# Optimization experiments

Measured on AMD Instinct MI355X. Metric: run time of the kernel, lower is better.

The kernel has to match this reference:

```python
import jax, jax.numpy as jnp
import numpy as np

B, C, H, W = 8, 320, 32, 32
HEADS, DHEAD = 8, 40
CTX_LEN, CTX_DIM = 77, 768
FF_INNER = 4 * C
GROUPS = 32
HW = H * W


def setup_inputs() -> dict:
    key = jax.random.key(0)
    ks = jax.random.split(key, 16)
    def nrm(k, shape, s=0.02):
        return (jax.random.normal(k, shape) * s).astype(jnp.float32)
    z = lambda *s: jnp.zeros(s, jnp.float32)
    o = lambda *s: jnp.ones(s, jnp.float32)
    inp = {}
    inp["x"] = jax.random.normal(ks[0], (B, C, H, W), jnp.float32)
    inp["context"] = jax.random.normal(ks[1], (B, CTX_LEN, CTX_DIM), jnp.float32)
    inp["vis_mask"] = jax.random.uniform(ks[2], (B, HW, HW)) > 0.5
    inp["v2t_mask"] = jax.random.uniform(ks[3], (B, HW, CTX_LEN)) > 0.5
    inp["gn_scale"] = o(C); inp["gn_bias"] = z(C)
    inp["proj_in_w"] = nrm(ks[4], (C, C)); inp["proj_in_b"] = z(C)
    inp["n1_s"] = o(C); inp["n1_b"] = z(C)
    inp["wq1"] = nrm(ks[5], (C, C)); inp["wk1"] = nrm(ks[6], (C, C)); inp["wv1"] = nrm(ks[7], (C, C))
    inp["wo1"] = nrm(ks[8], (C, C)); inp["bo1"] = z(C)
    inp["n2_s"] = o(C); inp["n2_b"] = z(C)
    inp["wq2"] = nrm(ks[9], (C, C)); inp["wk2"] = nrm(ks[10], (CTX_DIM, C)); inp["wv2"] = nrm(ks[11], (CTX_DIM, C))
    inp["wo2"] = nrm(ks[12], (C, C)); inp["bo2"] = z(C)
    inp["n3_s"] = o(C); inp["n3_b"] = z(C)
    inp["ff_w1"] = nrm(ks[13], (C, 2 * FF_INNER)); inp["ff_b1"] = z(2 * FF_INNER)
    inp["ff_w2"] = nrm(ks[14], (FF_INNER, C)); inp["ff_b2"] = z(C)
    inp["proj_out_w"] = nrm(ks[15], (C, C)); inp["proj_out_b"] = z(C)
    return inp


def group_norm(x, scale, bias, eps=1e-6):
    b, c, h, w = x.shape
    xg = x.reshape(b, GROUPS, -1)
    mu = xg.mean(-1, keepdims=True)
    var = xg.var(-1, keepdims=True)
    xn = ((xg - mu) * jax.lax.rsqrt(var + eps)).reshape(b, c, h, w)
    return xn * scale[None, :, None, None] + bias[None, :, None, None]


def layer_norm(x, s, b, eps=1e-5):
    mu = x.mean(-1, keepdims=True)
    var = x.var(-1, keepdims=True)
    return (x - mu) * jax.lax.rsqrt(var + eps) * s + b


def mha(xq, ctx, wq, wk, wv, wo, bo, mask):
    # CrossAttention: manual einsum softmax with boolean mask broadcast over heads
    b, n, _ = xq.shape
    m = ctx.shape[1]
    split = lambda t: t.reshape(b, -1, HEADS, DHEAD).transpose(0, 2, 1, 3)
    q = split(xq @ wq)   # [b,h,n,d]
    k = split(ctx @ wk)  # [b,h,m,d]
    v = split(ctx @ wv)
    sim = jnp.einsum('bhid,bhjd->bhij', q, k) * (DHEAD ** -0.5)
    if mask is not None:
        sim = jnp.where(mask[:, None, :, :], sim, jnp.finfo(sim.dtype).min)
    attn = jax.nn.softmax(sim, axis=-1)
    out = jnp.einsum('bhij,bhjd->bhid', attn, v)
    out = out.transpose(0, 2, 1, 3).reshape(b, n, HEADS * DHEAD)
    return out @ wo + bo


def reference(x, context, vis_mask, v2t_mask, gn_scale, gn_bias, proj_in_w, proj_in_b,
              n1_s, n1_b, wq1, wk1, wv1, wo1, bo1,
              n2_s, n2_b, wq2, wk2, wv2, wo2, bo2,
              n3_s, n3_b, ff_w1, ff_b1, ff_w2, ff_b2,
              proj_out_w, proj_out_b):
    x_in = x
    h = group_norm(x, gn_scale, gn_bias)
    # 1x1 conv proj_in == per-pixel linear; flatten b c h w -> b (hw) c
    h = h.reshape(B, C, HW).transpose(0, 2, 1) @ proj_in_w + proj_in_b
    # masked self-attention (vis mask)
    h = h + mha(layer_norm(h, n1_s, n1_b), layer_norm(h, n1_s, n1_b),
                wq1, wk1, wv1, wo1, bo1, vis_mask)
    # masked cross-attention to text (v2t mask)
    h = h + mha(layer_norm(h, n2_s, n2_b), context,
                wq2, wk2, wv2, wo2, bo2, v2t_mask)
    # GEGLU feedforward (glu=True, mult=4)
    y = layer_norm(h, n3_s, n3_b) @ ff_w1 + ff_b1
    a, g = jnp.split(y, 2, axis=-1)
    h = h + (a * jax.nn.gelu(g, approximate=False)) @ ff_w2 + ff_b2
    # proj_out + residual
    out = (h @ proj_out_w + proj_out_b).transpose(0, 2, 1).reshape(B, C, H, W)
    return out + x_in
```

## Files before the change

kernel.cpp:

```cpp
#include <hip/hip_runtime.h>
#include <hip/hip_bf16.h>
#include <math.h>


#define Bsz   8
#define Cch   320
#define HW    1024
#define NTOK  (Bsz*HW)
#define HEADS 8
#define DHEAD 40
#define CTXL  77
#define CTXD  768
#define FFI   1280
#define MCTX  (Bsz*CTXL)
#define MCTXP 640

typedef unsigned short u16;
typedef unsigned long long u64;
typedef __attribute__((ext_vector_type(8))) u16    u16x8;
typedef __attribute__((ext_vector_type(8))) __bf16 bf16x8;
typedef __attribute__((ext_vector_type(4))) float  f32x4;

__device__ inline u16 f2b(float f) {
    unsigned u = __float_as_uint(f);
    return (u16)((u + 0x7FFFu + ((u >> 16) & 1u)) >> 16);
}

__global__ __launch_bounds__(256) void gn_stats(
    const float* __restrict__ x, const float* __restrict__ scale,
    const float* __restrict__ bias, float* __restrict__ gnA,
    float* __restrict__ gnB)
{
    int blk = blockIdx.x;
    int b = blk >> 5, g = blk & 31;
    int tid = threadIdx.x;
    __shared__ float rs[256], rq[256];
    const float4* xg = (const float4*)(x + ((size_t)b*Cch + g*10)*HW);
    float s = 0.f, q = 0.f;
    #pragma unroll
    for (int i = 0; i < 10; ++i) {
        float4 v = xg[tid + i*256];
        s += v.x + v.y + v.z + v.w;
        q += v.x*v.x + v.y*v.y + v.z*v.z + v.w*v.w;
    }
    rs[tid] = s; rq[tid] = q; __syncthreads();
    for (int off = 128; off > 0; off >>= 1) {
        if (tid < off) { rs[tid] += rs[tid+off]; rq[tid] += rq[tid+off]; }
        __syncthreads();
    }
    if (tid < 10) {
        float mean = rs[0] * (1.f/10240.f);
        float var  = rq[0] * (1.f/10240.f) - mean*mean;
        float inv  = rsqrtf(var + 1e-6f);
        int ch = g*10 + tid;
        float a = inv * scale[ch];
        gnA[b*Cch + ch] = a;
        gnB[b*Cch + ch] = bias[ch] - mean*a;
    }
}

__global__ __launch_bounds__(256) void gn_apply(
    const float* __restrict__ x, const float* __restrict__ gnA,
    const float* __restrict__ gnB, u16* __restrict__ out)
{
    __shared__ u16 T[64*72];
    const int tid = threadIdx.x;
    const int c0 = blockIdx.x * 64;
    const int p0 = blockIdx.y * 64;
    const int b  = blockIdx.z;
    for (int e = tid; e < 512; e += 256) {
        int r = e >> 3, ch = e & 7;
        const float* src = x + ((size_t)(b*Cch + c0 + r))*HW + p0 + ch*8;
        float a  = gnA[b*Cch + c0 + r];
        float bb = gnB[b*Cch + c0 + r];
        float4 v0 = *(const float4*)src;
        float4 v1 = *(const float4*)(src + 4);
        u16x8 val;
        val[0] = f2b(v0.x*a + bb); val[1] = f2b(v0.y*a + bb);
        val[2] = f2b(v0.z*a + bb); val[3] = f2b(v0.w*a + bb);
        val[4] = f2b(v1.x*a + bb); val[5] = f2b(v1.y*a + bb);
        val[6] = f2b(v1.z*a + bb); val[7] = f2b(v1.w*a + bb);
        *(u16x8*)&T[r*72 + (ch ^ (r & 7))*8] = val;
    }
    __syncthreads();
    for (int e = tid; e < 4096; e += 256) {
        int p = e >> 6, c = e & 63;
        u16 v = T[c*72 + (((p >> 3) ^ (c & 7))*8) + (p & 7)];
        out[((size_t)(b*HW + p0 + p))*Cch + c0 + c] = v;
    }
}

__global__ __launch_bounds__(256) void layernorm_kernel(
    const float* __restrict__ in, const float* __restrict__ s,
    const float* __restrict__ bgain, u16* __restrict__ out)
{
    int t = blockIdx.x*4 + (threadIdx.x >> 6);
    int lane = threadIdx.x & 63;
    const float* row = in + (size_t)t*Cch;
    float v[5];
    float sum = 0.f, sq = 0.f;
    #pragma unroll
    for (int i = 0; i < 5; ++i) {
        v[i] = row[lane + 64*i];
        sum += v[i]; sq += v[i]*v[i];
    }
    #pragma unroll
    for (int off = 32; off > 0; off >>= 1) {
        sum += __shfl_xor(sum, off);
        sq  += __shfl_xor(sq,  off);
    }
    float mean = sum * (1.f/320.f);
    float var  = sq  * (1.f/320.f) - mean*mean;
    float inv  = rsqrtf(var + 1e-5f);
    u16* orow = out + (size_t)t*Cch;
    #pragma unroll
    for (int i = 0; i < 5; ++i) {
        int c = lane + 64*i;
        orow[c] = f2b((v[i]-mean)*inv*s[c] + bgain[c]);
    }
}

struct WDesc { const float* src; u16* dst; int K; int N; int nelem; float scl; };
struct WPack { WDesc w[12]; };

__global__ __launch_bounds__(256) void convert_weights(WPack p, int total)
{
    int idx = blockIdx.x*256 + threadIdx.x;
    if (idx >= total) return;
    #pragma unroll
    for (int i = 0; i < 12; ++i) {
        if (idx < p.w[i].nelem) {
            int K = p.w[i].K, N = p.w[i].N;
            int n = idx / K, k = idx - n*K;
            p.w[i].dst[(size_t)n*K + k] = f2b(p.w[i].src[(size_t)k*N + n] * p.w[i].scl);
            return;
        }
        idx -= p.w[i].nelem;
    }
}

__global__ __launch_bounds__(256) void convert_ctx(
    const float* __restrict__ src, u16* __restrict__ dst)
{
    int idx = blockIdx.x*256 + threadIdx.x;
    if (idx >= MCTXP*CTXD) return;
    int r = idx / CTXD;
    float v = (r < MCTX) ? src[idx] : 0.f;
    dst[idx] = f2b(v);
}

__global__ __launch_bounds__(256) void gemm_bf16(
    const u16* __restrict__ A, const u16* __restrict__ Wt,
    const float* __restrict__ bias, const float* __restrict__ res,
    float* __restrict__ out, u16* __restrict__ out_bf, int M, int N, int K)
{
    __shared__ u16 As[128*40];
    __shared__ u16 Bs[64*40];
    const int tid  = threadIdx.x;
    const int lane = tid & 63;
    const int w    = tid >> 6;
    const int m0   = blockIdx.y * 128;
    const int n0   = blockIdx.x * 64;
    const int fr   = lane & 15, fg = lane >> 4;
    const int ar   = tid >> 2, ac = tid & 3;

    const u16* pa0 = A  + (size_t)(m0 + ar)*K      + ac*8;
    const u16* pa1 = A  + (size_t)(m0 + ar + 64)*K + ac*8;
    const u16* pb  = Wt + (size_t)(n0 + ar)*K      + ac*8;
    u16x8 ra0 = *(const u16x8*)pa0;
    u16x8 ra1 = *(const u16x8*)pa1;
    u16x8 rb  = *(const u16x8*)pb;

    f32x4 acc[2][4] = {};
    for (int k0 = 0; k0 < K; k0 += 32) {
        *(u16x8*)&As[ar*40 + ac*8]      = ra0;
        *(u16x8*)&As[(ar+64)*40 + ac*8] = ra1;
        *(u16x8*)&Bs[ar*40 + ac*8]      = rb;
        __syncthreads();
        if (k0 + 32 < K) {
            pa0 += 32; pa1 += 32; pb += 32;
            ra0 = *(const u16x8*)pa0;
            ra1 = *(const u16x8*)pa1;
            rb  = *(const u16x8*)pb;
        }
        bf16x8 a0 = *(const bf16x8*)&As[(w*32      + fr)*40 + fg*8];
        bf16x8 a1 = *(const bf16x8*)&As[(w*32 + 16 + fr)*40 + fg*8];
        #pragma unroll
        for (int nt = 0; nt < 4; ++nt) {
            bf16x8 b = *(const bf16x8*)&Bs[(nt*16 + fr)*40 + fg*8];
            acc[0][nt] = __builtin_amdgcn_mfma_f32_16x16x32_bf16(a0, b, acc[0][nt], 0, 0, 0);
            acc[1][nt] = __builtin_amdgcn_mfma_f32_16x16x32_bf16(a1, b, acc[1][nt], 0, 0, 0);
        }
        __syncthreads();
    }
    #pragma unroll
    for (int at = 0; at < 2; ++at) {
        #pragma unroll
        for (int nt = 0; nt < 4; ++nt) {
            int gn = n0 + nt*16 + fr;
            float bv = bias ? bias[gn] : 0.f;
            #pragma unroll
            for (int i = 0; i < 4; ++i) {
                int gm = m0 + w*32 + at*16 + fg*4 + i;
                float v = acc[at][nt][i] + bv;
                if (res) v += res[(size_t)gm*N + gn];
                if (out) out[(size_t)gm*N + gn] = v;
                if (out_bf) out_bf[(size_t)gm*N + gn] = f2b(v);
            }
        }
    }
}

__global__ __launch_bounds__(256) void gemm_pout(
    const u16* __restrict__ A, const u16* __restrict__ Wt,
    const float* __restrict__ bias, const float* __restrict__ x,
    float* __restrict__ out, int K)
{
    __shared__ u16 As[128*40];
    __shared__ u16 Bs[64*40];
    const int tid  = threadIdx.x;
    const int lane = tid & 63;
    const int w    = tid >> 6;
    const int m0   = blockIdx.y * 128;
    const int n0   = blockIdx.x * 64;
    const int fr   = lane & 15, fg = lane >> 4;
    const int ar   = tid >> 2, ac = tid & 3;

    const u16* pa0 = A  + (size_t)(m0 + ar)*K      + ac*8;
    const u16* pa1 = A  + (size_t)(m0 + ar + 64)*K + ac*8;
    const u16* pb  = Wt + (size_t)(n0 + ar)*K      + ac*8;
    u16x8 ra0 = *(const u16x8*)pa0;
    u16x8 ra1 = *(const u16x8*)pa1;
    u16x8 rb  = *(const u16x8*)pb;

    f32x4 acc[2][4] = {};
    for (int k0 = 0; k0 < K; k0 += 32) {
        *(u16x8*)&As[ar*40 + ac*8]      = ra0;
        *(u16x8*)&As[(ar+64)*40 + ac*8] = ra1;
        *(u16x8*)&Bs[ar*40 + ac*8]      = rb;
        __syncthreads();
        if (k0 + 32 < K) {
            pa0 += 32; pa1 += 32; pb += 32;
            ra0 = *(const u16x8*)pa0;
            ra1 = *(const u16x8*)pa1;
            rb  = *(const u16x8*)pb;
        }
        bf16x8 a0 = *(const bf16x8*)&As[(w*32      + fr)*40 + fg*8];
        bf16x8 a1 = *(const bf16x8*)&As[(w*32 + 16 + fr)*40 + fg*8];
        #pragma unroll
        for (int nt = 0; nt < 4; ++nt) {
            bf16x8 b = *(const bf16x8*)&Bs[(nt*16 + fr)*40 + fg*8];
            acc[0][nt] = __builtin_amdgcn_mfma_f32_16x16x32_bf16(a0, b, acc[0][nt], 0, 0, 0);
            acc[1][nt] = __builtin_amdgcn_mfma_f32_16x16x32_bf16(a1, b, acc[1][nt], 0, 0, 0);
        }
        __syncthreads();
    }
    #pragma unroll
    for (int at = 0; at < 2; ++at) {
        #pragma unroll
        for (int nt = 0; nt < 4; ++nt) {
            int gn = n0 + nt*16 + fr;
            float bv = bias[gn];
            int gm0 = m0 + w*32 + at*16 + fg*4;
            int b   = gm0 >> 10;
            int p   = gm0 & (HW-1);
            size_t o = ((size_t)(b*Cch + gn))*HW + p;
            f32x4 xv = *(const f32x4*)&x[o];
            f32x4 vv;
            #pragma unroll
            for (int i = 0; i < 4; ++i) vv[i] = acc[at][nt][i] + bv + xv[i];
            *(f32x4*)&out[o] = vv;
        }
    }
}

__global__ __launch_bounds__(256) void ctx_kv_gemm(
    const u16* __restrict__ ctx, const u16* __restrict__ wk,
    const u16* __restrict__ wv, u16* __restrict__ kout, u16* __restrict__ vout)
{
    __shared__ u16 As[64*40];
    __shared__ u16 Bs[64*40];
    const int tid  = threadIdx.x;
    const int lane = tid & 63;
    const int w    = tid >> 6;
    const int m0   = blockIdx.y * 64;
    const int n0   = blockIdx.x * 64;
    const u16* Wt  = blockIdx.z ? wv : wk;
    u16* outp      = blockIdx.z ? vout : kout;
    const int fr   = lane & 15, fg = lane >> 4;
    const int ar   = tid >> 2, ac = tid & 3;

    const u16* pa = ctx + (size_t)(m0 + ar)*CTXD + ac*8;
    const u16* pb = Wt  + (size_t)(n0 + ar)*CTXD + ac*8;
    u16x8 ra = *(const u16x8*)pa;
    u16x8 rb = *(const u16x8*)pb;

    f32x4 acc[4] = {};
    for (int k0 = 0; k0 < CTXD; k0 += 32) {
        *(u16x8*)&As[ar*40 + ac*8] = ra;
        *(u16x8*)&Bs[ar*40 + ac*8] = rb;
        __syncthreads();
        if (k0 + 32 < CTXD) {
            pa += 32; pb += 32;
            ra = *(const u16x8*)pa;
            rb = *(const u16x8*)pb;
        }
        bf16x8 a = *(const bf16x8*)&As[(w*16 + fr)*40 + fg*8];
        #pragma unroll
        for (int nt = 0; nt < 4; ++nt) {
            bf16x8 b = *(const bf16x8*)&Bs[(nt*16 + fr)*40 + fg*8];
            acc[nt] = __builtin_amdgcn_mfma_f32_16x16x32_bf16(a, b, acc[nt], 0, 0, 0);
        }
        __syncthreads();
    }
    #pragma unroll
    for (int nt = 0; nt < 4; ++nt) {
        int gn = n0 + nt*16 + fr;
        #pragma unroll
        for (int i = 0; i < 4; ++i) {
            int gm = m0 + w*16 + fg*4 + i;
            if (gm < MCTX)
                outp[(size_t)gm*Cch + gn] = f2b(acc[nt][i]);
        }
    }
}

__global__ __launch_bounds__(256) void geglu_bf16(
    const u16* __restrict__ A, const u16* __restrict__ Wt,
    const float* __restrict__ b1, u16* __restrict__ out, int M, int K)
{
    __shared__ u16 As[128*40];
    __shared__ u16 Ba[64*40];
    __shared__ u16 Bg[64*40];
    const int tid  = threadIdx.x;
    const int lane = tid & 63;
    const int w    = tid >> 6;
    const int m0   = blockIdx.y * 128;
    const int n0   = blockIdx.x * 64;
    const int fr   = lane & 15, fg = lane >> 4;
    const int ar   = tid >> 2, ac = tid & 3;

    const u16* pa0 = A  + (size_t)(m0 + ar)*K      + ac*8;
    const u16* pa1 = A  + (size_t)(m0 + ar + 64)*K + ac*8;
    const u16* pba = Wt + (size_t)(n0 + ar)*K       + ac*8;
    const u16* pbg = Wt + (size_t)(FFI + n0 + ar)*K + ac*8;
    u16x8 ra0 = *(const u16x8*)pa0;
    u16x8 ra1 = *(const u16x8*)pa1;
    u16x8 rba = *(const u16x8*)pba;
    u16x8 rbg = *(const u16x8*)pbg;

    f32x4 aca[2][4] = {}, acg[2][4] = {};
    for (int k0 = 0; k0 < K; k0 += 32) {
        *(u16x8*)&As[ar*40 + ac*8]      = ra0;
        *(u16x8*)&As[(ar+64)*40 + ac*8] = ra1;
        *(u16x8*)&Ba[ar*40 + ac*8]      = rba;
        *(u16x8*)&Bg[ar*40 + ac*8]      = rbg;
        __syncthreads();
        if (k0 + 32 < K) {
            pa0 += 32; pa1 += 32; pba += 32; pbg += 32;
            ra0 = *(const u16x8*)pa0;
            ra1 = *(const u16x8*)pa1;
            rba = *(const u16x8*)pba;
            rbg = *(const u16x8*)pbg;
        }
        bf16x8 a0 = *(const bf16x8*)&As[(w*32      + fr)*40 + fg*8];
        bf16x8 a1 = *(const bf16x8*)&As[(w*32 + 16 + fr)*40 + fg*8];
        #pragma unroll
        for (int nt = 0; nt < 4; ++nt) {
            bf16x8 ba = *(const bf16x8*)&Ba[(nt*16 + fr)*40 + fg*8];
            bf16x8 bg = *(const bf16x8*)&Bg[(nt*16 + fr)*40 + fg*8];
            aca[0][nt] = __builtin_amdgcn_mfma_f32_16x16x32_bf16(a0, ba, aca[0][nt], 0, 0, 0);
            aca[1][nt] = __builtin_amdgcn_mfma_f32_16x16x32_bf16(a1, ba, aca[1][nt], 0, 0, 0);
            acg[0][nt] = __builtin_amdgcn_mfma_f32_16x16x32_bf16(a0, bg, acg[0][nt], 0, 0, 0);
            acg[1][nt] = __builtin_amdgcn_mfma_f32_16x16x32_bf16(a1, bg, acg[1][nt], 0, 0, 0);
        }
        __syncthreads();
    }
    #pragma unroll
    for (int at = 0; at < 2; ++at) {
        #pragma unroll
        for (int nt = 0; nt < 4; ++nt) {
            int gn = n0 + nt*16 + fr;
            float ba = b1[gn], bg = b1[FFI + gn];
            #pragma unroll
            for (int i = 0; i < 4; ++i) {
                int gm = m0 + w*32 + at*16 + fg*4 + i;
                float av = aca[at][nt][i] + ba;
                float gv = acg[at][nt][i] + bg;
                float gel = 0.5f*gv*(1.f + erff(gv*0.70710678118654752f));
                out[(size_t)gm*FFI + gn] = f2b(av*gel);
            }
        }
    }
}

__global__ __launch_bounds__(256) void transpose_v(
    const u16* __restrict__ in, int istride, u16* __restrict__ out,
    int Ltok, int ostride)
{
    __shared__ u16 T[64*72];
    const int tid = threadIdx.x;
    const int c0 = blockIdx.x * 64;
    const int t0 = blockIdx.y * 64;
    const int b  = blockIdx.z;
    for (int e = tid; e < 512; e += 256) {
        int r = e >> 3, ch = e & 7;
        u16x8 val = {};
        if (t0 + r < Ltok)
            val = *(const u16x8*)(in + ((size_t)(b*Ltok + t0 + r))*istride + c0 + ch*8);
        *(u16x8*)&T[r*72 + (ch ^ (r & 7))*8] = val;
    }
    __syncthreads();
    for (int e = tid; e < 4096; e += 256) {
        int c = e >> 6, t = e & 63;
        u16 v = T[t*72 + (((c >> 3) ^ (t & 7))*8) + (c & 7)];
        out[((size_t)(b*Cch + c0 + c))*ostride + t0 + t] = v;
    }
}

__global__ void detect_mask_kernel(const unsigned char* __restrict__ m, int* flag)
{
    __shared__ int any;
    if (threadIdx.x == 0) any = 0;
    __syncthreads();
    for (int i = threadIdx.x; i < 4096; i += 256)
        if ((i & 3) && m[i]) any = 1;
    __syncthreads();
    if (threadIdx.x == 0) *flag = any;
}

__global__ __launch_bounds__(256) void mask_bits_kernel(
    const void* __restrict__ mask, const int* __restrict__ mflag,
    u64* __restrict__ bits, int Lkv, int nw)
{
    const int wv   = threadIdx.x >> 6;
    const int lane = threadIdx.x & 63;
    const int row  = blockIdx.x*4 + wv;
    const int isU8 = *mflag;
    const unsigned char* m8  = (const unsigned char*)mask;
    const int*           m32 = (const int*)mask;
    const size_t base = (size_t)row * Lkv;
    for (int w = 0; w < nw; ++w) {
        int j = w*64 + lane;
        bool on = (j < Lkv) && (isU8 ? (m8[base+j] != 0) : (m32[base+j] != 0));
        u64 word = __ballot(on);
        if (lane == 0) bits[(size_t)row*nw + w] = word;
    }
}

__global__ __launch_bounds__(256) void flash_mfma(
    const u16* __restrict__ qb, int qstride,
    const u16* __restrict__ kb, int kstride,
    const u16* __restrict__ vt, int vstride,
    const u64* __restrict__ mbits, int nw,
    u16* __restrict__ out,
    int Lkv)
{
    __shared__ u16 QPs[64*72];
    __shared__ u16 Ks[64*72];
    __shared__ u16 Vs[48*72];

    const int tid  = threadIdx.x;
    const int lane = tid & 63;
    const int w    = tid >> 6;
    const int col  = lane & 15;
    const int quad = lane >> 4;
    const int q0   = blockIdx.x * 64;
    const int h    = blockIdx.y;
    const int b    = blockIdx.z;
    const int ch   = tid & 7;
    const int r0   = tid >> 3;

    {
        const u16* qT = qb + ((size_t)(b*HW + q0))*qstride + (size_t)h*DHEAD + ch*8;
        u16x8 v0 = {}, v1 = {};
        if (ch < 5) {
            v0 = *(const u16x8*)(qT + (size_t)r0*qstride);
            v1 = *(const u16x8*)(qT + (size_t)(r0+32)*qstride);
        }
        *(u16x8*)&QPs[r0*72 + ch*8]      = v0;
        *(u16x8*)&QPs[(r0+32)*72 + ch*8] = v1;
    }
    __syncthreads();
    const bf16x8 qa0 = *(const bf16x8*)&QPs[(w*16 + col)*72 +  0 + quad*8];
    const bf16x8 qa1 = *(const bf16x8*)&QPs[(w*16 + col)*72 + 32 + quad*8];

    const u16* kT = kb + (size_t)b*Lkv*kstride + (size_t)h*DHEAD + ch*8;
    const bool kok = ch < 5;
    const u16* vT = vt + ((size_t)(b*Cch + h*DHEAD))*vstride + ch*8;
    const u64* mrow = mbits + ((size_t)(b*HW + q0 + w*16 + quad*4))*nw;

    f32x4 acc_o[3] = {};

    const int nkt = (Lkv + 63) / 64;
    for (int jt = 0; jt < nkt; ++jt) {
        const int j0 = jt*64;
        __syncthreads();
        {
            u16x8 v0 = {}, v1 = {};
            if (kok) {
                if (j0 + r0      < Lkv) v0 = *(const u16x8*)(kT + (size_t)(j0 + r0)*kstride);
                if (j0 + r0 + 32 < Lkv) v1 = *(const u16x8*)(kT + (size_t)(j0 + r0 + 32)*kstride);
            }
            *(u16x8*)&Ks[r0*72 + ch*8]      = v0;
            *(u16x8*)&Ks[(r0+32)*72 + ch*8] = v1;
        }
        {
            u16x8 v0 = {};
            if (r0 < DHEAD) v0 = *(const u16x8*)(vT + (size_t)r0*vstride + j0);
            *(u16x8*)&Vs[r0*72 + ch*8] = v0;
            if (tid < 128) {
                int d1 = 32 + (tid >> 3);
                u16x8 v1 = {};
                if (d1 < DHEAD) v1 = *(const u16x8*)(vT + (size_t)d1*vstride + j0);
                else if (d1 == DHEAD) {
                    #pragma unroll
                    for (int z = 0; z < 8; ++z) v1[z] = 0x3F80;
                }
                *(u16x8*)&Vs[d1*72 + ch*8] = v1;
            }
        }
        __syncthreads();

        u64 mw[4];
        #pragma unroll
        for (int i = 0; i < 4; ++i) mw[i] = mrow[i*nw + jt];

        f32x4 s[4] = {};
        #pragma unroll
        for (int nt = 0; nt < 4; ++nt) {
            bf16x8 b0 = *(const bf16x8*)&Ks[(nt*16 + col)*72 +  0 + quad*8];
            bf16x8 b1 = *(const bf16x8*)&Ks[(nt*16 + col)*72 + 32 + quad*8];
            s[nt] = __builtin_amdgcn_mfma_f32_16x16x32_bf16(qa0, b0, s[nt], 0, 0, 0);
            s[nt] = __builtin_amdgcn_mfma_f32_16x16x32_bf16(qa1, b1, s[nt], 0, 0, 0);
        }

        #pragma unroll
        for (int i = 0; i < 4; ++i) {
            #pragma unroll
            for (int nt = 0; nt < 4; ++nt) {
                float p = __expf(s[nt][i]);
                unsigned bits = (unsigned)(mw[i] >> (nt*16));
                s[nt][i] = ((bits >> col) & 1u) ? p : 0.f;
            }
        }

        #pragma unroll
        for (int nt = 0; nt < 4; ++nt)
            #pragma unroll
            for (int i = 0; i < 4; ++i)
                QPs[(w*16 + quad*4 + i)*68 + nt*16 + col] =
                    (u16)(__float_as_uint(s[nt][i]) >> 16);

        bf16x8 pa0, pa1;
        __builtin_memcpy(&pa0, &QPs[(w*16 + col)*68 +  0 + quad*8], 16);
        __builtin_memcpy(&pa1, &QPs[(w*16 + col)*68 + 32 + quad*8], 16);
        #pragma unroll
        for (int nt = 0; nt < 3; ++nt) {
            bf16x8 vb0 = *(const bf16x8*)&Vs[(nt*16 + col)*72 +  0 + quad*8];
            bf16x8 vb1 = *(const bf16x8*)&Vs[(nt*16 + col)*72 + 32 + quad*8];
            acc_o[nt] = __builtin_amdgcn_mfma_f32_16x16x32_bf16(pa0, vb0, acc_o[nt], 0, 0, 0);
            acc_o[nt] = __builtin_amdgcn_mfma_f32_16x16x32_bf16(pa1, vb1, acc_o[nt], 0, 0, 0);
        }
    }

    float inv_l[4];
    #pragma unroll
    for (int i = 0; i < 4; ++i)
        inv_l[i] = 1.f / __shfl(acc_o[2][i], (lane & 48) | 8);

    #pragma unroll
    for (int nt = 0; nt < 3; ++nt) {
        int d = nt*16 + col;
        if (d < DHEAD) {
            #pragma unroll
            for (int i = 0; i < 4; ++i) {
                int q = q0 + w*16 + quad*4 + i;
                out[((size_t)(b*HW + q))*Cch + h*DHEAD + d] = f2b(acc_o[nt][i] * inv_l[i]);
            }
        }
    }
}

extern "C" void kernel_launch(void* const* d_in, const int* in_sizes, int n_in,
                              void* d_out, int out_size, void* d_ws, size_t ws_size,
                              hipStream_t stream)
{
    const float* x        = (const float*)d_in[0];
    const float* context  = (const float*)d_in[1];
    const void*  vis_mask = d_in[2];
    const void*  v2t_mask = d_in[3];
    const float* gn_s     = (const float*)d_in[4];
    const float* gn_b     = (const float*)d_in[5];
    const float* proj_in_w= (const float*)d_in[6];
    const float* proj_in_b= (const float*)d_in[7];
    const float* n1_s     = (const float*)d_in[8];
    const float* n1_b     = (const float*)d_in[9];
    const float* wq1      = (const float*)d_in[10];
    const float* wk1      = (const float*)d_in[11];
    const float* wv1      = (const float*)d_in[12];
    const float* wo1      = (const float*)d_in[13];
    const float* bo1      = (const float*)d_in[14];
    const float* n2_s     = (const float*)d_in[15];
    const float* n2_b     = (const float*)d_in[16];
    const float* wq2      = (const float*)d_in[17];
    const float* wk2      = (const float*)d_in[18];
    const float* wv2      = (const float*)d_in[19];
    const float* wo2      = (const float*)d_in[20];
    const float* bo2      = (const float*)d_in[21];
    const float* n3_s     = (const float*)d_in[22];
    const float* n3_b     = (const float*)d_in[23];
    const float* ff_w1    = (const float*)d_in[24];
    const float* ff_b1    = (const float*)d_in[25];
    const float* ff_w2    = (const float*)d_in[26];
    const float* ff_b2    = (const float*)d_in[27];
    const float* pout_w   = (const float*)d_in[28];
    const float* pout_b   = (const float*)d_in[29];
    float* out = (float*)d_out;

    const size_t TOKC = (size_t)NTOK*Cch;
    float* ws   = (float*)d_ws;
    float* Hb   = ws;
    u16*   QKV  = (u16*)(Hb + TOKC);
    u16*   Vt_g = QKV + 3*TOKC;
    u16*   G_bf = QKV;
    u16*   T0b  = Vt_g + TOKC;
    u16*   T1b  = T0b + TOKC;
    u16*   Hb_bf= T1b + TOKC;
    u16*   Wbf  = Hb_bf + TOKC;
    int*   mfl    = (int*)(Wbf + 2539520);
    u64*   mb_vis = (u64*)(Wbf + 2539528);
    u64*   mb_v2t = mb_vis + 131072;
    u16*   ctx_bf = (u16*)(mb_v2t + 16384);
    u16*   Kc_bf  = ctx_bf + MCTXP*CTXD;
    u16*   Vc_bf  = Kc_bf + 640*Cch;
    float* gnA    = (float*)(Vc_bf + 640*Cch);
    float* gnB    = gnA + Bsz*Cch;

    u16* w_q1  = Wbf;
    u16* w_k1  = Wbf +  102400;
    u16* w_v1  = Wbf +  204800;
    u16* w_pin = Wbf +  307200;
    u16* w_o1  = Wbf +  409600;
    u16* w_q2  = Wbf +  512000;
    u16* w_o2  = Wbf +  614400;
    u16* w_ff1 = Wbf +  716800;
    u16* w_ff2 = Wbf + 1536000;
    u16* w_po  = Wbf + 1945600;
    u16* w_k2  = Wbf + 2048000;
    u16* w_v2  = Wbf + 2293760;

    const float scale = 0.15811388300841897f;
    WPack pack;
    pack.w[0]  = { wq1,       w_q1,  Cch, Cch, Cch*Cch, scale };
    pack.w[1]  = { wk1,       w_k1,  Cch, Cch, Cch*Cch, 1.f };
    pack.w[2]  = { wv1,       w_v1,  Cch, Cch, Cch*Cch, 1.f };
    pack.w[3]  = { proj_in_w, w_pin, Cch, Cch, Cch*Cch, 1.f };
    pack.w[4]  = { wo1,       w_o1,  Cch, Cch, Cch*Cch, 1.f };
    pack.w[5]  = { wq2,       w_q2,  Cch, Cch, Cch*Cch, scale };
    pack.w[6]  = { wo2,       w_o2,  Cch, Cch, Cch*Cch, 1.f };
    pack.w[7]  = { ff_w1,     w_ff1, Cch, 2*FFI, Cch*2*FFI, 1.f };
    pack.w[8]  = { ff_w2,     w_ff2, FFI, Cch, FFI*Cch, 1.f };
    pack.w[9]  = { pout_w,    w_po,  Cch, Cch, Cch*Cch, 1.f };
    pack.w[10] = { wk2,       w_k2,  CTXD, Cch, CTXD*Cch, 1.f };
    pack.w[11] = { wv2,       w_v2,  CTXD, Cch, CTXD*Cch, 1.f };
    int wtotal = 0;
    for (int i = 0; i < 12; ++i) wtotal += pack.w[i].nelem;

    dim3 blk256(256);
    dim3 gTok(Cch/64, NTOK/128);
    dim3 gQKV(960/64, NTOK/128);
    dim3 gKV(Cch/64, MCTXP/64, 2);
    dim3 gFF(FFI/64, NTOK/128);
    dim3 gFA(HW/64, HEADS, Bsz);
    dim3 gTrS(Cch/64, HW/64, Bsz);
    dim3 gTrX(Cch/64, 2, Bsz);
    dim3 gGN(Cch/64, HW/64, Bsz);

    detect_mask_kernel<<<1, blk256, 0, stream>>>((const unsigned char*)vis_mask, mfl);
    mask_bits_kernel<<<NTOK/4, blk256, 0, stream>>>(vis_mask, mfl, mb_vis, HW, 16);
    mask_bits_kernel<<<NTOK/4, blk256, 0, stream>>>(v2t_mask, mfl, mb_v2t, CTXL, 2);
    convert_weights<<<(wtotal + 255)/256, blk256, 0, stream>>>(pack, wtotal);
    convert_ctx<<<(MCTXP*CTXD + 255)/256, blk256, 0, stream>>>(context, ctx_bf);

    gn_stats<<<Bsz*32, blk256, 0, stream>>>(x, gn_s, gn_b, gnA, gnB);
    gn_apply<<<gGN, blk256, 0, stream>>>(x, gnA, gnB, T0b);
    gemm_bf16<<<gTok, blk256, 0, stream>>>(T0b, w_pin, proj_in_b, nullptr, Hb, nullptr, NTOK, Cch, Cch);

    layernorm_kernel<<<NTOK/4, blk256, 0, stream>>>(Hb, n1_s, n1_b, T0b);
    gemm_bf16<<<gQKV, blk256, 0, stream>>>(T0b, w_q1, nullptr, nullptr, nullptr, QKV, NTOK, 960, Cch);
    transpose_v<<<gTrS, blk256, 0, stream>>>(QKV + 640, 960, Vt_g, HW, HW);
    flash_mfma<<<gFA, blk256, 0, stream>>>(QKV, 960, QKV + 320, 960, Vt_g, HW,
                                           mb_vis, 16, T1b, HW);
    gemm_bf16<<<gTok, blk256, 0, stream>>>(T1b, w_o1, bo1, Hb, Hb, nullptr, NTOK, Cch, Cch);

    layernorm_kernel<<<NTOK/4, blk256, 0, stream>>>(Hb, n2_s, n2_b, T0b);
    gemm_bf16<<<gTok, blk256, 0, stream>>>(T0b, w_q2, nullptr, nullptr, nullptr, QKV, NTOK, Cch, Cch);
    ctx_kv_gemm<<<gKV, blk256, 0, stream>>>(ctx_bf, w_k2, w_v2, Kc_bf, Vc_bf);
    transpose_v<<<gTrX, blk256, 0, stream>>>(Vc_bf, Cch, Vt_g, CTXL, 128);
    flash_mfma<<<gFA, blk256, 0, stream>>>(QKV, Cch, Kc_bf, Cch, Vt_g, 128,
                                           mb_v2t, 2, T1b, CTXL);
    gemm_bf16<<<gTok, blk256, 0, stream>>>(T1b, w_o2, bo2, Hb, Hb, nullptr, NTOK, Cch, Cch);

    layernorm_kernel<<<NTOK/4, blk256, 0, stream>>>(Hb, n3_s, n3_b, T0b);
    geglu_bf16<<<gFF, blk256, 0, stream>>>(T0b, w_ff1, ff_b1, G_bf, NTOK, Cch);
    gemm_bf16<<<gTok, blk256, 0, stream>>>(G_bf, w_ff2, ff_b2, Hb, nullptr, Hb_bf, NTOK, Cch, FFI);

    gemm_pout<<<gTok, blk256, 0, stream>>>(Hb_bf, w_po, pout_b, x, out, Cch);
}
```

Baseline: 424.2 us.

## Fuse preprocessing kernels into one launch and double-buffer GEMM shared tiles

Merges mask detection, mask bit-packing, weight conversion and context conversion into a single preamble kernel. Each mask block now re-probes the mask dtype itself, so the separate detect kernel and its flag buffer go away. All GEMM kernels (generic, proj_out, ctx KV, GEGLU) now use double-buffered LDS tiles, which removes one __syncthreads per k-step and overlaps tile stores with MFMA. This doubles shared memory per block, which may reduce occupancy.

```diff
diff --git a/kernel.cpp b/kernel.cpp
--- a/kernel.cpp
+++ b/kernel.cpp
@@ -123,30 +123,61 @@
 struct WDesc { const float* src; u16* dst; int K; int N; int nelem; float scl; };
 struct WPack { WDesc w[12]; };
 
-__global__ __launch_bounds__(256) void convert_weights(WPack p, int total)
-{
-    int idx = blockIdx.x*256 + threadIdx.x;
-    if (idx >= total) return;
-    #pragma unroll
-    for (int i = 0; i < 12; ++i) {
-        if (idx < p.w[i].nelem) {
-            int K = p.w[i].K, N = p.w[i].N;
-            int n = idx / K, k = idx - n*K;
-            p.w[i].dst[(size_t)n*K + k] = f2b(p.w[i].src[(size_t)k*N + n] * p.w[i].scl);
-            return;
-        }
-        idx -= p.w[i].nelem;
-    }
-}
-
-__global__ __launch_bounds__(256) void convert_ctx(
-    const float* __restrict__ src, u16* __restrict__ dst)
-{
-    int idx = blockIdx.x*256 + threadIdx.x;
-    if (idx >= MCTXP*CTXD) return;
-    int r = idx / CTXD;
-    float v = (r < MCTX) ? src[idx] : 0.f;
-    dst[idx] = f2b(v);
+#define WBLK 9920
+#define CBLK 1920
+
+__global__ __launch_bounds__(256) void preamble(
+    WPack p, const float* __restrict__ ctxsrc, u16* __restrict__ ctxdst,
+    const void* __restrict__ vis, const void* __restrict__ v2t,
+    u64* __restrict__ bvis, u64* __restrict__ bv2t)
+{
+    int blk = blockIdx.x;
+    int tid = threadIdx.x;
+    if (blk < WBLK) {
+        int idx = blk*256 + tid;
+        #pragma unroll
+        for (int i = 0; i < 12; ++i) {
+            if (idx < p.w[i].nelem) {
+                int K = p.w[i].K, N = p.w[i].N;
+                int n = idx / K, k = idx - n*K;
+                p.w[i].dst[(size_t)n*K + k] =
+                    f2b(p.w[i].src[(size_t)k*N + n] * p.w[i].scl);
+                return;
+            }
+            idx -= p.w[i].nelem;
+        }
+        return;
+    }
+    if (blk < WBLK + CBLK) {
+        int idx = (blk - WBLK)*256 + tid;
+        int r = idx / CTXD;
+        float v = (r < MCTX) ? ctxsrc[idx] : 0.f;
+        ctxdst[idx] = f2b(v);
+        return;
+    }
+    __shared__ int any;
+    if (tid == 0) any = 0;
+    __syncthreads();
+    const unsigned char* probe = (const unsigned char*)vis;
+    for (int i = tid; i < 4096; i += 256)
+        if ((i & 3) && probe[i]) any = 1;
+    __syncthreads();
+    const int isU8 = any;
+    int mb = blk - WBLK - CBLK;
+    const void* mask; u64* bits; int Lkv, nw;
+    if (mb < 2048) { mask = vis; bits = bvis; Lkv = HW;   nw = 16; }
+    else           { mask = v2t; bits = bv2t; Lkv = CTXL; nw = 2; mb -= 2048; }
+    const int wv = tid >> 6, lane = tid & 63;
+    const int row = mb*4 + wv;
+    const unsigned char* m8  = (const unsigned char*)mask;
+    const int*           m32 = (const int*)mask;
+    const size_t base = (size_t)row * Lkv;
+    for (int w = 0; w < nw; ++w) {
+        int j = w*64 + lane;
+        bool on = (j < Lkv) && (isU8 ? (m8[base+j] != 0) : (m32[base+j] != 0));
+        u64 word = __ballot(on);
+        if (lane == 0) bits[(size_t)row*nw + w] = word;
+    }
 }
 
 __global__ __launch_bounds__(256) void gemm_bf16(
@@ -154,8 +185,8 @@
     const float* __restrict__ bias, const float* __restrict__ res,
     float* __restrict__ out, u16* __restrict__ out_bf, int M, int N, int K)
 {
-    __shared__ u16 As[128*40];
-    __shared__ u16 Bs[64*40];
+    __shared__ u16 As[2][128*40];
+    __shared__ u16 Bs[2][64*40];
     const int tid  = threadIdx.x;
     const int lane = tid & 63;
     const int w    = tid >> 6;
@@ -167,31 +198,42 @@
     const u16* pa0 = A  + (size_t)(m0 + ar)*K      + ac*8;
     const u16* pa1 = A  + (size_t)(m0 + ar + 64)*K + ac*8;
     const u16* pb  = Wt + (size_t)(n0 + ar)*K      + ac*8;
-    u16x8 ra0 = *(const u16x8*)pa0;
-    u16x8 ra1 = *(const u16x8*)pa1;
-    u16x8 rb  = *(const u16x8*)pb;
+    const int nk = K >> 5;
+
+    *(u16x8*)&As[0][ar*40 + ac*8]      = *(const u16x8*)pa0;
+    *(u16x8*)&As[0][(ar+64)*40 + ac*8] = *(const u16x8*)pa1;
+    *(u16x8*)&Bs[0][ar*40 + ac*8]      = *(const u16x8*)pb;
+    u16x8 ra0, ra1, rb;
+    if (nk > 1) {
+        pa0 += 32; pa1 += 32; pb += 32;
+        ra0 = *(const u16x8*)pa0;
+        ra1 = *(const u16x8*)pa1;
+        rb  = *(const u16x8*)pb;
+    }
 
     f32x4 acc[2][4] = {};
-    for (int k0 = 0; k0 < K; k0 += 32) {
-        *(u16x8*)&As[ar*40 + ac*8]      = ra0;
-        *(u16x8*)&As[(ar+64)*40 + ac*8] = ra1;
-        *(u16x8*)&Bs[ar*40 + ac*8]      = rb;
+    for (int i = 0; i < nk; ++i) {
         __syncthreads();
-        if (k0 + 32 < K) {
-            pa0 += 32; pa1 += 32; pb += 32;
-            ra0 = *(const u16x8*)pa0;
-            ra1 = *(const u16x8*)pa1;
-            rb  = *(const u16x8*)pb;
-        }
-        bf16x8 a0 = *(const bf16x8*)&As[(w*32      + fr)*40 + fg*8];
-        bf16x8 a1 = *(const bf16x8*)&As[(w*32 + 16 + fr)*40 + fg*8];
+        const int cur = i & 1;
+        if (i + 1 < nk) {
+            *(u16x8*)&As[cur^1][ar*40 + ac*8]      = ra0;
+            *(u16x8*)&As[cur^1][(ar+64)*40 + ac*8] = ra1;
+            *(u16x8*)&Bs[cur^1][ar*40 + ac*8]      = rb;
+            if (i + 2 < nk) {
+                pa0 += 32; pa1 += 32; pb += 32;
+                ra0 = *(const u16x8*)pa0;
+                ra1 = *(const u16x8*)pa1;
+                rb  = *(const u16x8*)pb;
+            }
+        }
+        bf16x8 a0 = *(const bf16x8*)&As[cur][(w*32      + fr)*40 + fg*8];
+        bf16x8 a1 = *(const bf16x8*)&As[cur][(w*32 + 16 + fr)*40 + fg*8];
         #pragma unroll
         for (int nt = 0; nt < 4; ++nt) {
-            bf16x8 b = *(const bf16x8*)&Bs[(nt*16 + fr)*40 + fg*8];
+            bf16x8 b = *(const bf16x8*)&Bs[cur][(nt*16 + fr)*40 + fg*8];
             acc[0][nt] = __builtin_amdgcn_mfma_f32_16x16x32_bf16(a0, b, acc[0][nt], 0, 0, 0);
             acc[1][nt] = __builtin_amdgcn_mfma_f32_16x16x32_bf16(a1, b, acc[1][nt], 0, 0, 0);
         }
-        __syncthreads();
     }
     #pragma unroll
     for (int at = 0; at < 2; ++at) {
@@ -216,8 +258,8 @@
     const float* __restrict__ bias, const float* __restrict__ x,
     float* __restrict__ out, int K)
 {
-    __shared__ u16 As[128*40];
-    __shared__ u16 Bs[64*40];
+    __shared__ u16 As[2][128*40];
+    __shared__ u16 Bs[2][64*40];
     const int tid  = threadIdx.x;
     const int lane = tid & 63;
     const int w    = tid >> 6;
@@ -229,31 +271,42 @@
     const u16* pa0 = A  + (size_t)(m0 + ar)*K      + ac*8;
     const u16* pa1 = A  + (size_t)(m0 + ar + 64)*K + ac*8;
     const u16* pb  = Wt + (size_t)(n0 + ar)*K      + ac*8;
-    u16x8 ra0 = *(const u16x8*)pa0;
-    u16x8 ra1 = *(const u16x8*)pa1;
-    u16x8 rb  = *(const u16x8*)pb;
+    const int nk = K >> 5;
+
+    *(u16x8*)&As[0][ar*40 + ac*8]      = *(const u16x8*)pa0;
+    *(u16x8*)&As[0][(ar+64)*40 + ac*8] = *(const u16x8*)pa1;
+    *(u16x8*)&Bs[0][ar*40 + ac*8]      = *(const u16x8*)pb;
+    u16x8 ra0, ra1, rb;
+    if (nk > 1) {
+        pa0 += 32; pa1 += 32; pb += 32;
+        ra0 = *(const u16x8*)pa0;
+        ra1 = *(const u16x8*)pa1;
+        rb  = *(const u16x8*)pb;
+    }
 
     f32x4 acc[2][4] = {};
-    for (int k0 = 0; k0 < K; k0 += 32) {
-        *(u16x8*)&As[ar*40 + ac*8]      = ra0;
-        *(u16x8*)&As[(ar+64)*40 + ac*8] = ra1;
-        *(u16x8*)&Bs[ar*40 + ac*8]      = rb;
+    for (int i = 0; i < nk; ++i) {
         __syncthreads();
-        if (k0 + 32 < K) {
-            pa0 += 32; pa1 += 32; pb += 32;
-            ra0 = *(const u16x8*)pa0;
-            ra1 = *(const u16x8*)pa1;
-            rb  = *(const u16x8*)pb;
-        }
-        bf16x8 a0 = *(const bf16x8*)&As[(w*32      + fr)*40 + fg*8];
-        bf16x8 a1 = *(const bf16x8*)&As[(w*32 + 16 + fr)*40 + fg*8];
+        const int cur = i & 1;
+        if (i + 1 < nk) {
+            *(u16x8*)&As[cur^1][ar*40 + ac*8]      = ra0;
+            *(u16x8*)&As[cur^1][(ar+64)*40 + ac*8] = ra1;
+            *(u16x8*)&Bs[cur^1][ar*40 + ac*8]      = rb;
+            if (i + 2 < nk) {
+                pa0 += 32; pa1 += 32; pb += 32;
+                ra0 = *(const u16x8*)pa0;
+                ra1 = *(const u16x8*)pa1;
+                rb  = *(const u16x8*)pb;
+            }
+        }
+        bf16x8 a0 = *(const bf16x8*)&As[cur][(w*32      + fr)*40 + fg*8];
+        bf16x8 a1 = *(const bf16x8*)&As[cur][(w*32 + 16 + fr)*40 + fg*8];
         #pragma unroll
         for (int nt = 0; nt < 4; ++nt) {
-            bf16x8 b = *(const bf16x8*)&Bs[(nt*16 + fr)*40 + fg*8];
+            bf16x8 b = *(const bf16x8*)&Bs[cur][(nt*16 + fr)*40 + fg*8];
             acc[0][nt] = __builtin_amdgcn_mfma_f32_16x16x32_bf16(a0, b, acc[0][nt], 0, 0, 0);
             acc[1][nt] = __builtin_amdgcn_mfma_f32_16x16x32_bf16(a1, b, acc[1][nt], 0, 0, 0);
         }
-        __syncthreads();
     }
     #pragma unroll
     for (int at = 0; at < 2; ++at) {
@@ -278,8 +331,8 @@
     const u16* __restrict__ ctx, const u16* __restrict__ wk,
     const u16* __restrict__ wv, u16* __restrict__ kout, u16* __restrict__ vout)
 {
-    __shared__ u16 As[64*40];
-    __shared__ u16 Bs[64*40];
+    __shared__ u16 As[2][64*40];
+    __shared__ u16 Bs[2][64*40];
     const int tid  = threadIdx.x;
     const int lane = tid & 63;
     const int w    = tid >> 6;
@@ -292,26 +345,34 @@
 
     const u16* pa = ctx + (size_t)(m0 + ar)*CTXD + ac*8;
     const u16* pb = Wt  + (size_t)(n0 + ar)*CTXD + ac*8;
-    u16x8 ra = *(const u16x8*)pa;
-    u16x8 rb = *(const u16x8*)pb;
+    const int nk = CTXD >> 5;
+
+    *(u16x8*)&As[0][ar*40 + ac*8] = *(const u16x8*)pa;
+    *(u16x8*)&Bs[0][ar*40 + ac*8] = *(const u16x8*)pb;
+    u16x8 ra, rb;
+    pa += 32; pb += 32;
+    ra = *(const u16x8*)pa;
+    rb = *(const u16x8*)pb;
 
     f32x4 acc[4] = {};
-    for (int k0 = 0; k0 < CTXD; k0 += 32) {
-        *(u16x8*)&As[ar*40 + ac*8] = ra;
-        *(u16x8*)&Bs[ar*40 + ac*8] = rb;
+    for (int i = 0; i < nk; ++i) {
         __syncthreads();
-        if (k0 + 32 < CTXD) {
-            pa += 32; pb += 32;
-            ra = *(const u16x8*)pa;
-            rb = *(const u16x8*)pb;
-        }
-        bf16x8 a = *(const bf16x8*)&As[(w*16 + fr)*40 + fg*8];
+        const int cur = i & 1;
+        if (i + 1 < nk) {
+            *(u16x8*)&As[cur^1][ar*40 + ac*8] = ra;
+            *(u16x8*)&Bs[cur^1][ar*40 + ac*8] = rb;
+            if (i + 2 < nk) {
+                pa += 32; pb += 32;
+                ra = *(const u16x8*)pa;
+                rb = *(const u16x8*)pb;
+            }
+        }
+        bf16x8 a = *(const bf16x8*)&As[cur][(w*16 + fr)*40 + fg*8];
         #pragma unroll
         for (int nt = 0; nt < 4; ++nt) {
-            bf16x8 b = *(const bf16x8*)&Bs[(nt*16 + fr)*40 + fg*8];
+            bf16x8 b = *(const bf16x8*)&Bs[cur][(nt*16 + fr)*40 + fg*8];
             acc[nt] = __builtin_amdgcn_mfma_f32_16x16x32_bf16(a, b, acc[nt], 0, 0, 0);
         }
-        __syncthreads();
     }
     #pragma unroll
     for (int nt = 0; nt < 4; ++nt) {
@@ -329,9 +390,9 @@
     const u16* __restrict__ A, const u16* __restrict__ Wt,
     const float* __restrict__ b1, u16* __restrict__ out, int M, int K)
 {
-    __shared__ u16 As[128*40];
-    __shared__ u16 Ba[64*40];
-    __shared__ u16 Bg[64*40];
+    __shared__ u16 As[2][128*40];
+    __shared__ u16 Ba[2][64*40];
+    __shared__ u16 Bg[2][64*40];
     const int tid  = threadIdx.x;
     const int lane = tid & 63;
     const int w    = tid >> 6;
@@ -344,37 +405,49 @@
     const u16* pa1 = A  + (size_t)(m0 + ar + 64)*K + ac*8;
     const u16* pba = Wt + (size_t)(n0 + ar)*K       + ac*8;
     const u16* pbg = Wt + (size_t)(FFI + n0 + ar)*K + ac*8;
-    u16x8 ra0 = *(const u16x8*)pa0;
-    u16x8 ra1 = *(const u16x8*)pa1;
-    u16x8 rba = *(const u16x8*)pba;
-    u16x8 rbg = *(const u16x8*)pbg;
+    const int nk = K >> 5;
+
+    *(u16x8*)&As[0][ar*40 + ac*8]      = *(const u16x8*)pa0;
+    *(u16x8*)&As[0][(ar+64)*40 + ac*8] = *(const u16x8*)pa1;
+    *(u16x8*)&Ba[0][ar*40 + ac*8]      = *(const u16x8*)pba;
+    *(u16x8*)&Bg[0][ar*40 + ac*8]      = *(const u16x8*)pbg;
+    u16x8 ra0, ra1, rba, rbg;
+    if (nk > 1) {
+        pa0 += 32; pa1 += 32; pba += 32; pbg += 32;
+        ra0 = *(const u16x8*)pa0;
+        ra1 = *(const u16x8*)pa1;
+        rba = *(const u16x8*)pba;
+        rbg = *(const u16x8*)pbg;
+    }
 
     f32x4 aca[2][4] = {}, acg[2][4] = {};
-    for (int k0 = 0; k0 < K; k0 += 32) {
-        *(u16x8*)&As[ar*40 + ac*8]      = ra0;
-        *(u16x8*)&As[(ar+64)*40 + ac*8] = ra1;
-        *(u16x8*)&Ba[ar*40 + ac*8]      = rba;
-        *(u16x8*)&Bg[ar*40 + ac*8]      = rbg;
+    for (int i = 0; i < nk; ++i) {
         __syncthreads();
-        if (k0 + 32 < K) {
-            pa0 += 32; pa1 += 32; pba += 32; pbg += 32;
-            ra0 = *(const u16x8*)pa0;
-            ra1 = *(const u16x8*)pa1;
-            rba = *(const u16x8*)pba;
-            rbg = *(const u16x8*)pbg;
-        }
-        bf16x8 a0 = *(const bf16x8*)&As[(w*32      + fr)*40 + fg*8];
-        bf16x8 a1 = *(const bf16x8*)&As[(w*32 + 16 + fr)*40 + fg*8];
+        const int cur = i & 1;
+        if (i + 1 < nk) {
+            *(u16x8*)&As[cur^1][ar*40 + ac*8]      = ra0;
+            *(u16x8*)&As[cur^1][(ar+64)*40 + ac*8] = ra1;
+            *(u16x8*)&Ba[cur^1][ar*40 + ac*8]      = rba;
+            *(u16x8*)&Bg[cur^1][ar*40 + ac*8]      = rbg;
+            if (i + 2 < nk) {
+                pa0 += 32; pa1 += 32; pba += 32; pbg += 32;
+                ra0 = *(const u16x8*)pa0;
+                ra1 = *(const u16x8*)pa1;
+                rba = *(const u16x8*)pba;
+                rbg = *(const u16x8*)pbg;
+            }
+        }
+        bf16x8 a0 = *(const bf16x8*)&As[cur][(w*32      + fr)*40 + fg*8];
+        bf16x8 a1 = *(const bf16x8*)&As[cur][(w*32 + 16 + fr)*40 + fg*8];
         #pragma unroll
         for (int nt = 0; nt < 4; ++nt) {
-            bf16x8 ba = *(const bf16x8*)&Ba[(nt*16 + fr)*40 + fg*8];
-            bf16x8 bg = *(const bf16x8*)&Bg[(nt*16 + fr)*40 + fg*8];
+            bf16x8 ba = *(const bf16x8*)&Ba[cur][(nt*16 + fr)*40 + fg*8];
+            bf16x8 bg = *(const bf16x8*)&Bg[cur][(nt*16 + fr)*40 + fg*8];
             aca[0][nt] = __builtin_amdgcn_mfma_f32_16x16x32_bf16(a0, ba, aca[0][nt], 0, 0, 0);
             aca[1][nt] = __builtin_amdgcn_mfma_f32_16x16x32_bf16(a1, ba, aca[1][nt], 0, 0, 0);
             acg[0][nt] = __builtin_amdgcn_mfma_f32_16x16x32_bf16(a0, bg, acg[0][nt], 0, 0, 0);
             acg[1][nt] = __builtin_amdgcn_mfma_f32_16x16x32_bf16(a1, bg, acg[1][nt], 0, 0, 0);
         }
-        __syncthreads();
     }
     #pragma unroll
     for (int at = 0; at < 2; ++at) {
@@ -415,36 +488,6 @@
         int c = e >> 6, t = e & 63;
         u16 v = T[t*72 + (((c >> 3) ^ (t & 7))*8) + (c & 7)];
         out[((size_t)(b*Cch + c0 + c))*ostride + t0 + t] = v;
-    }
-}
-
-__global__ void detect_mask_kernel(const unsigned char* __restrict__ m, int* flag)
-{
-    __shared__ int any;
-    if (threadIdx.x == 0) any = 0;
-    __syncthreads();
-    for (int i = threadIdx.x; i < 4096; i += 256)
-        if ((i & 3) && m[i]) any = 1;
-    __syncthreads();
-    if (threadIdx.x == 0) *flag = any;
-}
-
-__global__ __launch_bounds__(256) void mask_bits_kernel(
-    const void* __restrict__ mask, const int* __restrict__ mflag,
-    u64* __restrict__ bits, int Lkv, int nw)
-{
-    const int wv   = threadIdx.x >> 6;
-    const int lane = threadIdx.x & 63;
-    const int row  = blockIdx.x*4 + wv;
-    const int isU8 = *mflag;
-    const unsigned char* m8  = (const unsigned char*)mask;
-    const int*           m32 = (const int*)mask;
-    const size_t base = (size_t)row * Lkv;
-    for (int w = 0; w < nw; ++w) {
-        int j = w*64 + lane;
-        bool on = (j < Lkv) && (isU8 ? (m8[base+j] != 0) : (m32[base+j] != 0));
-        u64 word = __ballot(on);
-        if (lane == 0) bits[(size_t)row*nw + w] = word;
     }
 }
 
@@ -628,8 +671,7 @@
     u16*   T1b  = T0b + TOKC;
     u16*   Hb_bf= T1b + TOKC;
     u16*   Wbf  = Hb_bf + TOKC;
-    int*   mfl    = (int*)(Wbf + 2539520);
-    u64*   mb_vis = (u64*)(Wbf + 2539528);
+    u64*   mb_vis = (u64*)(Wbf + 2539520);
     u64*   mb_v2t = mb_vis + 131072;
     u16*   ctx_bf = (u16*)(mb_v2t + 16384);
     u16*   Kc_bf  = ctx_bf + MCTXP*CTXD;
@@ -664,8 +706,6 @@
     pack.w[9]  = { pout_w,    w_po,  Cch, Cch, Cch*Cch, 1.f };
     pack.w[10] = { wk2,       w_k2,  CTXD, Cch, CTXD*Cch, 1.f };
     pack.w[11] = { wv2,       w_v2,  CTXD, Cch, CTXD*Cch, 1.f };
-    int wtotal = 0;
-    for (int i = 0; i < 12; ++i) wtotal += pack.w[i].nelem;
 
     dim3 blk256(256);
     dim3 gTok(Cch/64, NTOK/128);
@@ -677,11 +717,8 @@
     dim3 gTrX(Cch/64, 2, Bsz);
     dim3 gGN(Cch/64, HW/64, Bsz);
 
-    detect_mask_kernel<<<1, blk256, 0, stream>>>((const unsigned char*)vis_mask, mfl);
-    mask_bits_kernel<<<NTOK/4, blk256, 0, stream>>>(vis_mask, mfl, mb_vis, HW, 16);
-    mask_bits_kernel<<<NTOK/4, blk256, 0, stream>>>(v2t_mask, mfl, mb_v2t, CTXL, 2);
-    convert_weights<<<(wtotal + 255)/256, blk256, 0, stream>>>(pack, wtotal);
-    convert_ctx<<<(MCTXP*CTXD + 255)/256, blk256, 0, stream>>>(context, ctx_bf);
+    preamble<<<WBLK + CBLK + 4096, blk256, 0, stream>>>(
+        pack, context, ctx_bf, vis_mask, v2t_mask, mb_vis, mb_v2t);
 
     gn_stats<<<Bsz*32, blk256, 0, stream>>>(x, gn_s, gn_b, gnA, gnB);
     gn_apply<<<gGN, blk256, 0, stream>>>(x, gnA, gnB, T0b);
```

New measurement: 408.1 us. 1.04x faster.
